# Optimization experiments

Hardware: AMD Instinct MI355X
Metric: run time of the kernel (lower is better)

## Reference

```python
import jax, jax.numpy as jnp
import numpy as np

B, K, H, I, O, N_UNFOLDS = 256, 256, 128, 64, 64, 6
RESAMPLE_THRESHOLD = 0.5


def setup_inputs() -> dict:
    key = jax.random.key(0)
    ks = jax.random.split(key, 12)
    return {
        "x": jax.random.normal(ks[0], (B, I), dtype=jnp.float32),
        "particles": 0.1 * jax.random.normal(ks[1], (B, K, H), dtype=jnp.float32),
        "log_weights": jnp.zeros((B, K), dtype=jnp.float32),  # normalized to -log K inside
        "noise": jax.random.normal(ks[2], (B * K, N_UNFOLDS, H), dtype=jnp.float32),
        "resample_u": jax.random.uniform(ks[3], (B, K), dtype=jnp.float32),
        "Wx": 0.05 * jax.random.normal(ks[4], (I, H), dtype=jnp.float32),
        "Wh": 0.05 * jax.random.normal(ks[5], (H, H), dtype=jnp.float32),
        "b": jnp.zeros((H,), dtype=jnp.float32),
        "log_sigma": jnp.full((H,), -2.25, dtype=jnp.float32),  # softplus(-2.25) ~ 0.1 = sigma_init
        "W_out": 0.05 * jax.random.normal(ks[6], (H, O), dtype=jnp.float32),
        "b_out": jnp.zeros((O,), dtype=jnp.float32),
        "alpha_logit": jnp.zeros((), dtype=jnp.float32),  # sigmoid -> alpha_init = 0.5
    }


def reference(x, particles, log_weights, noise, resample_u,
              Wx, Wh, b, log_sigma, W_out, b_out, alpha_logit):
    Bv, Kv, Hv = particles.shape
    dt = 1.0 / N_UNFOLDS          # timespans=None -> elapsed_time = 1
    sqrt_dt = jnp.sqrt(jnp.asarray(dt, particles.dtype))
    g = jax.nn.softplus(log_sigma)  # learned state-independent diffusion [H]

    # --- propagate particles through Euler-Maruyama SDE ---
    s0 = particles.reshape(Bv * Kv, Hv)                 # [BK, H]
    x_exp = jnp.repeat(x, Kv, axis=0)                   # [BK, I] (expand along K)
    xWx = x_exp @ Wx + b                                # hoist input projection

    def em_step(s, eps):
        drift = jnp.tanh(xWx + s @ Wh) - s              # f(h, x)
        s = s + drift * dt + g * sqrt_dt * eps          # dh = f dt + g dW
        return s, None

    s, _ = jax.lax.scan(em_step, s0, jnp.swapaxes(noise, 0, 1))  # scan over n_unfolds
    new_particles = s.reshape(Bv, Kv, Hv)
    outputs = (s @ W_out + b_out).reshape(Bv, Kv, -1)   # [B, K, O]

    # --- soft resampling ---
    lw = log_weights - jax.nn.logsumexp(log_weights, axis=1, keepdims=True)
    w = jnp.exp(lw)                                     # [B, K]
    ess = 1.0 / jnp.sum(w * w, axis=1)                  # [B]
    alpha = jax.nn.sigmoid(alpha_logit)
    q = alpha * w + (1.0 - alpha) / Kv                  # proposal mixture
    cdf = jnp.cumsum(q, axis=1)
    idx = jax.vmap(jnp.searchsorted)(cdf, resample_u)   # inverse-CDF sampling [B, K]
    idx = jnp.clip(idx, 0, Kv - 1)
    gathered = jnp.take_along_axis(new_particles, idx[:, :, None], axis=1)
    lw_res = (jnp.take_along_axis(lw, idx, axis=1)
              - jnp.log(jnp.take_along_axis(q, idx, axis=1)))
    lw_res = lw_res - jax.nn.logsumexp(lw_res, axis=1, keepdims=True)
    need = (ess < RESAMPLE_THRESHOLD * Kv)[:, None]     # per-batch resample mask
    final_particles = jnp.where(need[:, :, None], gathered, new_particles)
    final_lw = jnp.where(need, lw_res, lw)

    # --- weighted average output ---
    weights = jnp.exp(final_lw - jax.nn.logsumexp(final_lw, axis=1, keepdims=True))
    output = jnp.sum(weights[:, :, None] * outputs, axis=1)  # [B, O]
    return output, final_particles, final_lw
```

## Files before the change

kernel.cpp:

```cpp
#include <hip/hip_runtime.h>
#include <math.h>

#define B_ 256
#define K_ 256
#define H_ 128
#define I_ 64
#define O_ 64
#define NU 6
#define BP 64
#define MW 16

typedef short bf16x8 __attribute__((ext_vector_type(8)));
typedef float f32x4  __attribute__((ext_vector_type(4)));

__device__ __forceinline__ unsigned short f2bf(float f) {
  unsigned int u = __builtin_bit_cast(unsigned int, f);
  unsigned int r = (u + 0x7FFFu + ((u >> 16) & 1u)) >> 16;
  return (unsigned short)r;
}

__device__ __forceinline__ unsigned int swz(unsigned int row, unsigned int col) {
  return (row * 256u + col * 2u) ^ ((row & 15u) << 4);
}

__device__ __forceinline__ float tanh_fast(float x) {
  float e = __expf(2.0f * x);
  return 1.0f - 2.0f * __builtin_amdgcn_rcpf(e + 1.0f);
}

__global__ __launch_bounds__(256) void prop_kernel(
    const float* __restrict__ x,
    const float* __restrict__ particles,
    const float* __restrict__ noise,
    const float* __restrict__ Wx,
    const float* __restrict__ Wh,
    const float* __restrict__ bvec,
    const float* __restrict__ log_sigma,
    float* __restrict__ p_out)
{
  __shared__ __align__(16) unsigned short whT[H_ * H_];
  __shared__ __align__(16) unsigned short sS[BP * H_];
  __shared__ __align__(16) float xwx[H_];
  __shared__ __align__(16) float gsd[H_];

  const int tid  = threadIdx.x;
  const int lane = tid & 63;
  const int wave = tid >> 6;
  const int bk0  = blockIdx.x * BP;
  const int b    = bk0 >> 8;
  const int lr   = lane & 15;
  const int lg   = lane >> 4;

  const int myp = bk0 + wave * MW + lr;
  const float* prow = particles + (size_t)myp * H_ + lg * 4;
  const float* nrow = noise + (size_t)myp * NU * H_ + lg * 4;
  float* orow = p_out + (size_t)myp * H_ + lg * 4;

  f32x4 s4[8], nA[8], nB[8], nC[8];
#pragma unroll
  for (int ct = 0; ct < 8; ++ct) s4[ct] = ((const f32x4*)prow)[ct * 4];
#pragma unroll
  for (int ct = 0; ct < 8; ++ct) nA[ct] = ((const f32x4*)nrow)[ct * 4];

#pragma unroll
  for (int it = 0; it < 16; ++it) {
    int idx = tid + it * 256;
    int k   = idx >> 5;
    int c0  = (idx & 31) * 4;
    float4 v = ((const float4*)Wh)[idx];
    float vv[4] = {v.x, v.y, v.z, v.w};
#pragma unroll
    for (int e = 0; e < 4; ++e)
      *(unsigned short*)((char*)whT + swz(c0 + e, k)) = f2bf(vv[e]);
  }
  if (tid < H_) {
    float acc = bvec[tid];
#pragma unroll 8
    for (int i = 0; i < I_; ++i) acc = fmaf(x[b * I_ + i], Wx[i * H_ + tid], acc);
    xwx[tid] = acc;
    gsd[tid] = log1pf(expf(log_sigma[tid])) * sqrtf(1.0f / 6.0f);
  }
  __syncthreads();

  const float dt = 1.0f / 6.0f;
  const int srow = wave * MW + lr;

#define LOADN(buf, n_) do {                                                  \
    const f32x4* np = (const f32x4*)(nrow + (size_t)(n_) * H_);              \
    _Pragma("unroll")                                                        \
    for (int ct = 0; ct < 8; ++ct) buf[ct] = np[ct * 4];                     \
  } while (0)

#define STEP(nb) do {                                                        \
    _Pragma("unroll")                                                        \
    for (int ct = 0; ct < 8; ++ct) {                                         \
      unsigned lo_ = (unsigned)f2bf(s4[ct][0]) | ((unsigned)f2bf(s4[ct][1]) << 16); \
      unsigned hi_ = (unsigned)f2bf(s4[ct][2]) | ((unsigned)f2bf(s4[ct][3]) << 16); \
      uint2 pk_ = {lo_, hi_};                                                \
      *(uint2*)((char*)sS + swz(srow, ct * 16 + lg * 4)) = pk_;              \
    }                                                                        \
    bf16x8 bfrag0 = *(const bf16x8*)((char*)sS + swz(srow, 0 * 32 + lg * 8));\
    bf16x8 bfrag1 = *(const bf16x8*)((char*)sS + swz(srow, 1 * 32 + lg * 8));\
    bf16x8 bfrag2 = *(const bf16x8*)((char*)sS + swz(srow, 2 * 32 + lg * 8));\
    bf16x8 bfrag3 = *(const bf16x8*)((char*)sS + swz(srow, 3 * 32 + lg * 8));\
    _Pragma("unroll")                                                        \
    for (int ct = 0; ct < 8; ++ct) {                                         \
      f32x4 acc = *(const f32x4*)&xwx[ct * 16 + lg * 4];                     \
      bf16x8 af0 = *(const bf16x8*)((char*)whT + swz(ct * 16 + lr, 0 * 32 + lg * 8)); \
      acc = __builtin_amdgcn_mfma_f32_16x16x32_bf16(af0, bfrag0, acc, 0, 0, 0); \
      bf16x8 af1 = *(const bf16x8*)((char*)whT + swz(ct * 16 + lr, 1 * 32 + lg * 8)); \
      acc = __builtin_amdgcn_mfma_f32_16x16x32_bf16(af1, bfrag1, acc, 0, 0, 0); \
      bf16x8 af2 = *(const bf16x8*)((char*)whT + swz(ct * 16 + lr, 2 * 32 + lg * 8)); \
      acc = __builtin_amdgcn_mfma_f32_16x16x32_bf16(af2, bfrag2, acc, 0, 0, 0); \
      bf16x8 af3 = *(const bf16x8*)((char*)whT + swz(ct * 16 + lr, 3 * 32 + lg * 8)); \
      acc = __builtin_amdgcn_mfma_f32_16x16x32_bf16(af3, bfrag3, acc, 0, 0, 0); \
      f32x4 gs = *(const f32x4*)&gsd[ct * 16 + lg * 4];                      \
      _Pragma("unroll")                                                      \
      for (int r = 0; r < 4; ++r) {                                          \
        float t_  = tanh_fast(acc[r]);                                       \
        float sv_ = s4[ct][r];                                               \
        s4[ct][r] = fmaf(t_ - sv_, dt, sv_) + gs[r] * nb[ct][r];             \
      }                                                                      \
    }                                                                        \
  } while (0)

  LOADN(nB, 1); LOADN(nC, 2);
  STEP(nA); LOADN(nA, 3);
  STEP(nB); LOADN(nB, 4);
  STEP(nC); LOADN(nC, 5);
  STEP(nA);
  STEP(nB);
  STEP(nC);

#undef LOADN
#undef STEP

#pragma unroll
  for (int ct = 0; ct < 8; ++ct) ((f32x4*)orow)[ct * 4] = s4[ct];
}

__device__ __forceinline__ float wave_sum(float v) {
#pragma unroll
  for (int off = 1; off < 64; off <<= 1) v += __shfl_xor(v, off, 64);
  return v;
}
__device__ __forceinline__ float wave_max(float v) {
#pragma unroll
  for (int off = 1; off < 64; off <<= 1) v = fmaxf(v, __shfl_xor(v, off, 64));
  return v;
}

__global__ __launch_bounds__(256) void finish_kernel(
  const float* __restrict__ log_weights,
  const float* __restrict__ resample_u,
  const float* __restrict__ W_out,
  const float* __restrict__ b_out,
  const float* __restrict__ alpha_logit,
  float* __restrict__ p,
  float* __restrict__ out0,
  float* __restrict__ lw_out)
{
  const int b = blockIdx.x, k = threadIdx.x;
  const int wv = k >> 6;
  __shared__ float red[K_];
  __shared__ float lw[K_], qv[K_], cdf[K_], wt[K_];
  __shared__ float ws_h[H_];
  __shared__ float warr[4];

#define BLK_SUM(dst, v) do {                                   \
    float pw_ = wave_sum(v);                                   \
    __syncthreads();                   \
    if ((k & 63) == 0) warr[wv] = pw_;                         \
    __syncthreads();                                           \
    dst = warr[0] + warr[1] + warr[2] + warr[3];               \
  } while (0)
#define BLK_MAX(dst, v) do {                                   \
    float pw_ = wave_max(v);                                   \
    __syncthreads();                                           \
    if ((k & 63) == 0) warr[wv] = pw_;                         \
    __syncthreads();                                           \
    dst = fmaxf(fmaxf(warr[0], warr[1]), fmaxf(warr[2], warr[3])); \
  } while (0)

  float lwk = log_weights[b*K_ + k];
  float mx;  BLK_MAX(mx, lwk);
  float se;  BLK_SUM(se, expf(lwk - mx));
  float lse = mx + logf(se);
  float lwn = lwk - lse;
  lw[k] = lwn;
  float w = expf(lwn);
  float sw2; BLK_SUM(sw2, w*w);
  float ess = 1.0f / sw2;

  float alpha = 1.0f/(1.0f + expf(-alpha_logit[0]));
  float qk = alpha*w + (1.0f-alpha)*(1.0f/K_);
  qv[k] = qk;
  cdf[k] = qk; __syncthreads();
  for (int off=1; off<K_; off<<=1){
    float add = (k>=off)? cdf[k-off] : 0.0f;
    __syncthreads();
    cdf[k] += add;
    __syncthreads();
  }
  float u = resample_u[b*K_ + k];
  int lo=0, cnt=K_;
  while (cnt>0){ int st=cnt>>1; if (cdf[lo+st] < u){ lo += st+1; cnt -= st+1; } else cnt = st; }
  int idx = min(lo, K_-1);

  float lr  = lw[idx] - logf(qv[idx]);
  float mx2; BLK_MAX(mx2, lr);
  float se2; BLK_SUM(se2, expf(lr-mx2));
  float lrn = lr - (mx2 + logf(se2));

  bool need = ess < 0.5f * K_;
  float flw = need ? lrn : lwn;
  lw_out[b*K_ + k] = flw;

  float mx3; BLK_MAX(mx3, flw);
  float se3; BLK_SUM(se3, expf(flw-mx3));
  float wk  = expf(flw - (mx3 + logf(se3)));
  wt[k] = wk;
  float sumw; BLK_SUM(sumw, wk);

#undef BLK_SUM
#undef BLK_MAX

  int h = k & (H_-1), half = k >> 7;
  float part = 0.f;
  const float* pb = &p[(size_t)b*K_*H_];
  for (int kk = half*128; kk < half*128 + 128; ++kk)
    part = fmaf(wt[kk], pb[(size_t)kk*H_ + h], part);
  red[k] = part; __syncthreads();
  if (k < H_) ws_h[k] = red[k] + red[k+H_];
  __syncthreads();

  if (k < O_) {
    float acc = sumw * b_out[k];
#pragma unroll 8
    for (int hh = 0; hh < H_; ++hh) acc = fmaf(ws_h[hh], W_out[hh*O_ + k], acc);
    out0[b*O_ + k] = acc;
  }

  if (need) {
    const float* src = &p[((size_t)b*K_ + idx)*H_];
    float* dstp      = &p[((size_t)b*K_ + k  )*H_];
    float tmp[16];
    for (int c = 0; c < H_; c += 16){
#pragma unroll
      for (int t=0;t<16;++t) tmp[t]=src[c+t];
      __syncthreads();
#pragma unroll
      for (int t=0;t<16;++t) dstp[c+t]=tmp[t];
      __syncthreads();
    }
  }
}

extern "C" void kernel_launch(void* const* d_in, const int* in_sizes, int n_in,
                              void* d_out, int out_size, void* d_ws, size_t ws_size,
                              hipStream_t stream) {
  const float* x           = (const float*)d_in[0];
  const float* particles   = (const float*)d_in[1];
  const float* log_weights = (const float*)d_in[2];
  const float* noise       = (const float*)d_in[3];
  const float* resample_u  = (const float*)d_in[4];
  const float* Wx          = (const float*)d_in[5];
  const float* Wh          = (const float*)d_in[6];
  const float* bvec        = (const float*)d_in[7];
  const float* log_sigma   = (const float*)d_in[8];
  const float* W_out       = (const float*)d_in[9];
  const float* b_out       = (const float*)d_in[10];
  const float* alpha_logit = (const float*)d_in[11];

  float* out0   = (float*)d_out;
  float* p_out  = out0 + B_*O_;
  float* lw_out = p_out + (size_t)B_*K_*H_;

  prop_kernel<<<(B_*K_)/BP, 256, 0, stream>>>(
      x, particles, noise, Wx, Wh, bvec, log_sigma, p_out);
  finish_kernel<<<B_, 256, 0, stream>>>(
      log_weights, resample_u, W_out, b_out, alpha_logit, p_out, out0, lw_out);
}
```

Before: 105.6 us.

## Stage noise through LDS with coalesced row loads and bf16 packing

Noise is now read by each wave as whole contiguous 512-byte rows instead of scattered 16-byte pieces per particle row. It is converted to bf16 and written to a new LDS buffer, and each step reads it back in the MFMA output layout. This targets the uncoalesced global noise traffic and replaces three register-resident noise buffers with one, which eases register pressure. The LDS swizzle also changes to xor on the low three row bits. The trade-offs are extra LDS footprint and traffic, and bf16 rounding of the noise.

```diff
diff --git a/kernel.cpp b/kernel.cpp
--- a/kernel.cpp
+++ b/kernel.cpp
@@ -13,14 +13,19 @@
 typedef short bf16x8 __attribute__((ext_vector_type(8)));
 typedef float f32x4  __attribute__((ext_vector_type(4)));
 
-__device__ __forceinline__ unsigned short f2bf(float f) {
+__device__ __forceinline__ unsigned int f2bf(float f) {
   unsigned int u = __builtin_bit_cast(unsigned int, f);
-  unsigned int r = (u + 0x7FFFu + ((u >> 16) & 1u)) >> 16;
-  return (unsigned short)r;
+  return (u + 0x7FFFu + ((u >> 16) & 1u)) >> 16;
+}
+__device__ __forceinline__ float bf2f_lo(unsigned int w) {
+  return __builtin_bit_cast(float, w << 16);
+}
+__device__ __forceinline__ float bf2f_hi(unsigned int w) {
+  return __builtin_bit_cast(float, w & 0xFFFF0000u);
 }
 
 __device__ __forceinline__ unsigned int swz(unsigned int row, unsigned int col) {
-  return (row * 256u + col * 2u) ^ ((row & 15u) << 4);
+  return (row * 256u + col * 2u) ^ ((row & 7u) << 4);
 }
 
 __device__ __forceinline__ float tanh_fast(float x) {
@@ -40,6 +45,7 @@
 {
   __shared__ __align__(16) unsigned short whT[H_ * H_];
   __shared__ __align__(16) unsigned short sS[BP * H_];
+  __shared__ __align__(16) unsigned short nz[BP * H_];
   __shared__ __align__(16) float xwx[H_];
   __shared__ __align__(16) float gsd[H_];
 
@@ -50,17 +56,36 @@
   const int b    = bk0 >> 8;
   const int lr   = lane & 15;
   const int lg   = lane >> 4;
+  const int hl   = lane >> 5;
+  const int cl   = lane & 31;
 
   const int myp = bk0 + wave * MW + lr;
   const float* prow = particles + (size_t)myp * H_ + lg * 4;
-  const float* nrow = noise + (size_t)myp * NU * H_ + lg * 4;
   float* orow = p_out + (size_t)myp * H_ + lg * 4;
-
-  f32x4 s4[8], nA[8], nB[8], nC[8];
+  const float* nzg = noise + (size_t)(bk0 + wave * MW) * NU * H_;
+
+  f32x4 s4[8], nzld[8];
+
+#define NLOAD(n_) do {                                                       \
+    _Pragma("unroll")                                                        \
+    for (int i = 0; i < 8; ++i)                                              \
+      nzld[i] = *(const f32x4*)(nzg + (size_t)(2*i + hl) * (NU*H_)           \
+                                + (size_t)(n_) * H_ + cl * 4);               \
+  } while (0)
+
+#define NWRITE() do {                                                        \
+    _Pragma("unroll")                                                        \
+    for (int i = 0; i < 8; ++i) {                                            \
+      unsigned lo_ = f2bf(nzld[i][0]) | (f2bf(nzld[i][1]) << 16);            \
+      unsigned hi_ = f2bf(nzld[i][2]) | (f2bf(nzld[i][3]) << 16);            \
+      uint2 pk_ = {lo_, hi_};                                                \
+      *(uint2*)((char*)nz + swz(wave * MW + 2*i + hl, cl * 4)) = pk_;        \
+    }                                                                        \
+  } while (0)
+
+  NLOAD(0);
 #pragma unroll
   for (int ct = 0; ct < 8; ++ct) s4[ct] = ((const f32x4*)prow)[ct * 4];
-#pragma unroll
-  for (int ct = 0; ct < 8; ++ct) nA[ct] = ((const f32x4*)nrow)[ct * 4];
 
 #pragma unroll
   for (int it = 0; it < 16; ++it) {
@@ -71,7 +96,7 @@
     float vv[4] = {v.x, v.y, v.z, v.w};
 #pragma unroll
     for (int e = 0; e < 4; ++e)
-      *(unsigned short*)((char*)whT + swz(c0 + e, k)) = f2bf(vv[e]);
+      *(unsigned short*)((char*)whT + swz(c0 + e, k)) = (unsigned short)f2bf(vv[e]);
   }
   if (tid < H_) {
     float acc = bvec[tid];
@@ -85,17 +110,11 @@
   const float dt = 1.0f / 6.0f;
   const int srow = wave * MW + lr;
 
-#define LOADN(buf, n_) do {                                                  \
-    const f32x4* np = (const f32x4*)(nrow + (size_t)(n_) * H_);              \
-    _Pragma("unroll")                                                        \
-    for (int ct = 0; ct < 8; ++ct) buf[ct] = np[ct * 4];                     \
-  } while (0)
-
-#define STEP(nb) do {                                                        \
+#define STEP() do {                                                          \
     _Pragma("unroll")                                                        \
     for (int ct = 0; ct < 8; ++ct) {                                         \
-      unsigned lo_ = (unsigned)f2bf(s4[ct][0]) | ((unsigned)f2bf(s4[ct][1]) << 16); \
-      unsigned hi_ = (unsigned)f2bf(s4[ct][2]) | ((unsigned)f2bf(s4[ct][3]) << 16); \
+      unsigned lo_ = f2bf(s4[ct][0]) | (f2bf(s4[ct][1]) << 16);              \
+      unsigned hi_ = f2bf(s4[ct][2]) | (f2bf(s4[ct][3]) << 16);              \
       uint2 pk_ = {lo_, hi_};                                                \
       *(uint2*)((char*)sS + swz(srow, ct * 16 + lg * 4)) = pk_;              \
     }                                                                        \
@@ -115,24 +134,36 @@
       bf16x8 af3 = *(const bf16x8*)((char*)whT + swz(ct * 16 + lr, 3 * 32 + lg * 8)); \
       acc = __builtin_amdgcn_mfma_f32_16x16x32_bf16(af3, bfrag3, acc, 0, 0, 0); \
       f32x4 gs = *(const f32x4*)&gsd[ct * 16 + lg * 4];                      \
-      _Pragma("unroll")                                                      \
-      for (int r = 0; r < 4; ++r) {                                          \
-        float t_  = tanh_fast(acc[r]);                                       \
-        float sv_ = s4[ct][r];                                               \
-        s4[ct][r] = fmaf(t_ - sv_, dt, sv_) + gs[r] * nb[ct][r];             \
-      }                                                                      \
+      uint2 nr = *(const uint2*)((char*)nz + swz(srow, ct * 16 + lg * 4));   \
+      float nv0 = bf2f_lo(nr.x), nv1 = bf2f_hi(nr.x);                        \
+      float nv2 = bf2f_lo(nr.y), nv3 = bf2f_hi(nr.y);                        \
+      float t0 = tanh_fast(acc[0]);                                          \
+      float t1 = tanh_fast(acc[1]);                                          \
+      float t2 = tanh_fast(acc[2]);                                          \
+      float t3 = tanh_fast(acc[3]);                                          \
+      s4[ct][0] = fmaf(t0 - s4[ct][0], dt, s4[ct][0]) + gs[0] * nv0;         \
+      s4[ct][1] = fmaf(t1 - s4[ct][1], dt, s4[ct][1]) + gs[1] * nv1;         \
+      s4[ct][2] = fmaf(t2 - s4[ct][2], dt, s4[ct][2]) + gs[2] * nv2;        \
+      s4[ct][3] = fmaf(t3 - s4[ct][3], dt, s4[ct][3]) + gs[3] * nv3;        \
     }                                                                        \
   } while (0)
 
-  LOADN(nB, 1); LOADN(nC, 2);
-  STEP(nA); LOADN(nA, 3);
-  STEP(nB); LOADN(nB, 4);
-  STEP(nC); LOADN(nC, 5);
-  STEP(nA);
-  STEP(nB);
-  STEP(nC);
-
-#undef LOADN
+  NWRITE();
+  NLOAD(1);
+  STEP();
+  NWRITE(); NLOAD(2);
+  STEP();
+  NWRITE(); NLOAD(3);
+  STEP();
+  NWRITE(); NLOAD(4);
+  STEP();
+  NWRITE(); NLOAD(5);
+  STEP();
+  NWRITE();
+  STEP();
+
+#undef NLOAD
+#undef NWRITE
 #undef STEP
 
 #pragma unroll
```

Result: slower. 132.6 us (+25.6%).
